# Kernel optimization log

Hardware: AMD Instinct MI355X
Metric: run time of the kernel (lower is better)

Reference implementation:

```python
import jax, jax.numpy as jnp
import numpy as np

NUM_HEADS = 8
DIM_HEAD = 48
SCALE = DIM_HEAD ** -0.5


def setup_inputs() -> dict:
    key = jax.random.key(0)
    k1, k2, k3 = jax.random.split(key, 3)
    B, N, D = 4, 2048, 384
    inner = NUM_HEADS * DIM_HEAD  # 384
    x = jax.random.normal(k1, (B, N, D), dtype=jnp.float32)
    # store weights in [in, out] layout (equivalent to torch Linear W.T)
    Wqkv = jax.random.normal(k2, (D, 3 * inner), dtype=jnp.float32) * (D ** -0.5)
    Wproj = jax.random.normal(k3, (inner, D), dtype=jnp.float32) * (inner ** -0.5)
    bproj = jnp.zeros((D,), dtype=jnp.float32)
    return {"x": x, "Wqkv": Wqkv, "Wproj": Wproj, "bproj": bproj}


def reference(x, Wqkv, Wproj, bproj):
    B, N, D = x.shape
    h, dh = NUM_HEADS, DIM_HEAD
    C = h * dh
    # fused QKV projection (qkv_bias=False)
    qkv = (x @ Wqkv).reshape(B, N, 3, h, dh)
    q = qkv[:, :, 0].transpose(0, 2, 1, 3)  # [B, h, N, dh]
    k = qkv[:, :, 1].transpose(0, 2, 1, 3)
    v = qkv[:, :, 2].transpose(0, 2, 1, 3)
    # naive attention: materialize [B, h, N, N] scores
    sim = jnp.einsum("bhqd,bhkd->bhqk", q, k) * SCALE
    attn = jax.nn.softmax(sim, axis=-1)
    out = jnp.einsum("bhqk,bhkd->bhqd", attn, v)  # [B, h, N, dh]
    out = out.transpose(0, 2, 1, 3).reshape(B, N, C)
    return out @ Wproj + bproj
```

## Files before the change

kernel.cpp:

```cpp
#include <hip/hip_runtime.h>
#include <hip/hip_bf16.h>


typedef _Float16 f16x8 __attribute__((ext_vector_type(8)));
typedef _Float16 f16x4 __attribute__((ext_vector_type(4)));
typedef float    f32x4 __attribute__((ext_vector_type(4)));
typedef float    f32x16 __attribute__((ext_vector_type(16)));

#define QSCL 0.20822035963448658f

__global__ __launch_bounds__(256) void prep(const float* __restrict__ wq,
                                            const float* __restrict__ wp,
                                            _Float16* __restrict__ wqt,
                                            _Float16* __restrict__ wpt)
{
    __shared__ _Float16 t[64][65];
    const int blk = blockIdx.x, tid = threadIdx.x;
    const float* src; _Float16* dst; int Nn, k0, n0;
    if (blk < 108) {
        src = wq; dst = wqt; Nn = 1152;
        k0 = (blk % 6) * 64; n0 = (blk / 6) * 64;
    } else {
        const int b2 = blk - 108;
        src = wp; dst = wpt; Nn = 384;
        k0 = (b2 % 6) * 64; n0 = (b2 / 6) * 64;
    }
    #pragma unroll
    for (int i = 0; i < 16; i++) {
        const int id = tid + i * 256;
        const int k = id >> 6, n = id & 63;
        t[k][n] = (_Float16)src[(size_t)(k0 + k) * Nn + n0 + n];
    }
    __syncthreads();
    #pragma unroll
    for (int i = 0; i < 16; i++) {
        const int id = tid + i * 256;
        const int n = id >> 6, k = id & 63;
        dst[(size_t)(n0 + n) * 384 + k0 + k] = t[k][n];
    }
}

union QkvSmem {
    struct { _Float16 As[128][72]; _Float16 Bs[64][72]; } g;
    _Float16 Ts[64][136];
};

__global__ __launch_bounds__(256) void qkv_f16(const float* __restrict__ X,
                                               const _Float16* __restrict__ Bt,
                                               _Float16* __restrict__ qh,
                                               _Float16* __restrict__ kh,
                                               _Float16* __restrict__ vt)
{
    __shared__ QkvSmem sm;
    const int tid = threadIdx.x;
    const int w = tid >> 6, lane = tid & 63, cl = lane & 15, quad = lane >> 4;
    const int bm = blockIdx.x, bn = blockIdx.y;

    f32x4 acc[2][4];
    const f32x4 z4 = {0.f, 0.f, 0.f, 0.f};
    #pragma unroll
    for (int mi = 0; mi < 2; mi++)
        #pragma unroll
        for (int t = 0; t < 4; t++) acc[mi][t] = z4;

    const int ar = tid >> 3, ac = (tid & 7) * 8;
    const float*    Ag = X  + (size_t)(bm * 128 + ar) * 384 + ac;
    const _Float16* Bg = Bt + (size_t)(bn * 64  + ar) * 384 + ac;

    float4 pa0[4], pa1[4];
    f16x8 pb[2];
    #pragma unroll
    for (int j = 0; j < 4; j++) {
        pa0[j] = *(const float4*)(Ag + (size_t)(32 * j) * 384);
        pa1[j] = *(const float4*)(Ag + (size_t)(32 * j) * 384 + 4);
    }
    #pragma unroll
    for (int j = 0; j < 2; j++) pb[j] = *(const f16x8*)(Bg + (size_t)(32 * j) * 384);

    for (int k0 = 0; k0 < 384; k0 += 64) {
        __syncthreads();
        #pragma unroll
        for (int j = 0; j < 4; j++) {
            f16x8 hh;
            hh[0] = (_Float16)pa0[j].x; hh[1] = (_Float16)pa0[j].y;
            hh[2] = (_Float16)pa0[j].z; hh[3] = (_Float16)pa0[j].w;
            hh[4] = (_Float16)pa1[j].x; hh[5] = (_Float16)pa1[j].y;
            hh[6] = (_Float16)pa1[j].z; hh[7] = (_Float16)pa1[j].w;
            *(f16x8*)&sm.g.As[ar + 32 * j][ac] = hh;
        }
        #pragma unroll
        for (int j = 0; j < 2; j++) *(f16x8*)&sm.g.Bs[ar + 32 * j][ac] = pb[j];
        __syncthreads();
        if (k0 + 64 < 384) {
            #pragma unroll
            for (int j = 0; j < 4; j++) {
                pa0[j] = *(const float4*)(Ag + (size_t)(32 * j) * 384 + k0 + 64);
                pa1[j] = *(const float4*)(Ag + (size_t)(32 * j) * 384 + k0 + 68);
            }
            #pragma unroll
            for (int j = 0; j < 2; j++)
                pb[j] = *(const f16x8*)(Bg + (size_t)(32 * j) * 384 + k0 + 64);
        }
        #pragma unroll
        for (int kh2 = 0; kh2 < 2; kh2++) {
            f16x8 bf[4];
            #pragma unroll
            for (int t = 0; t < 4; t++)
                bf[t] = *(const f16x8*)&sm.g.Bs[t * 16 + cl][kh2 * 32 + quad * 8];
            #pragma unroll
            for (int mi = 0; mi < 2; mi++) {
                const f16x8 af = *(const f16x8*)&sm.g.As[w * 32 + mi * 16 + cl][kh2 * 32 + quad * 8];
                #pragma unroll
                for (int t = 0; t < 4; t++)
                    acc[mi][t] = __builtin_amdgcn_mfma_f32_16x16x32_f16(af, bf[t], acc[mi][t], 0, 0, 0);
            }
        }
    }

    const int s = (bn * 64) / 384;
    if (s == 2) {
        __syncthreads();
        #pragma unroll
        for (int t = 0; t < 4; t++)
            #pragma unroll
            for (int mi = 0; mi < 2; mi++)
                #pragma unroll
                for (int r = 0; r < 4; r++)
                    sm.Ts[t * 16 + cl][w * 32 + mi * 16 + quad * 4 + r] =
                        (_Float16)acc[mi][t][r];
        __syncthreads();
        const int colbase = bn * 64 - 768;
        const int b  = (bm * 128) >> 11;
        const int n0 = (bm * 128) & 2047;
        #pragma unroll
        for (int i = 0; i < 4; i++) {
            const int c = i * 256 + tid;
            const int col = c >> 4, nc = c & 15;
            const int gcol = colbase + col;
            const int head = gcol / 48, d = gcol - head * 48;
            const int bh = b * 8 + head;
            *(f16x8*)&vt[(size_t)(bh * 48 + d) * 2048 + n0 + nc * 8] =
                *(const f16x8*)&sm.Ts[col][nc * 8];
        }
    } else {
        #pragma unroll
        for (int t = 0; t < 4; t++) {
            const int col  = bn * 64 + t * 16 + cl - s * 384;
            const int head = col / 48, d = col - head * 48;
            #pragma unroll
            for (int mi = 0; mi < 2; mi++) {
                #pragma unroll
                for (int r = 0; r < 4; r++) {
                    const int row = bm * 128 + w * 32 + mi * 16 + quad * 4 + r;
                    const int b = row >> 11, n = row & 2047;
                    const int bh = b * 8 + head;
                    const float v = acc[mi][t][r];
                    if (s == 0)
                        qh[(size_t)(bh * 2048 + n) * 48 + d] = (_Float16)(v * QSCL);
                    else
                        kh[(size_t)(bh * 2048 + n) * 48 + d] = (_Float16)v;
                }
            }
        }
    }
}

__global__ __launch_bounds__(256) void attn_f16(const _Float16* __restrict__ qh,
                                                const _Float16* __restrict__ kh,
                                                const _Float16* __restrict__ vt,
                                                _Float16* __restrict__ ab)
{
    __shared__ _Float16 Ks[64][56];
    __shared__ _Float16 Vts[64][72];
    __shared__ _Float16 Ps[128][72];
    const int tid = threadIdx.x;
    const int w = tid >> 6, lane = tid & 63, ln = lane & 31, h = lane >> 5;
    const int bh = blockIdx.x, qt = blockIdx.y;

    for (int i = tid; i < 16 * 72; i += 256) {
        const int r = 48 + i / 72, c = i - (i / 72) * 72;
        Vts[r][c] = (r == 48) ? (_Float16)1.0f : (_Float16)0.0f;
    }

    f16x8 qf[3];
    {
        const _Float16* qp = qh + (size_t)(bh * 2048 + qt * 128 + w * 32 + ln) * 48 + 8 * h;
        qf[0] = *(const f16x8*)qp;
        qf[1] = *(const f16x8*)(qp + 16);
        qf[2] = *(const f16x8*)(qp + 32);
    }

    f32x16 o0, o1;
    #pragma unroll
    for (int r = 0; r < 16; r++) { o0[r] = 0.f; o1[r] = 0.f; }

    const _Float16* kbase = kh + (size_t)bh * 2048 * 48;
    const _Float16* vbase = vt + (size_t)bh * 48 * 2048;

    const int kr0 = tid / 6,         kc0 = (tid % 6) * 8;
    const int kid1 = tid + 256;
    const int kr1 = kid1 / 6,        kc1 = (kid1 % 6) * 8;
    const int vr0 = tid >> 3,        vc0 = (tid & 7) * 8;
    const int vr1 = (tid + 256) >> 3;
    const _Float16* ks0 = kbase + (size_t)kr0 * 48 + kc0;
    const _Float16* ks1 = kbase + (size_t)kr1 * 48 + kc1;
    const _Float16* vs0 = vbase + (size_t)vr0 * 2048 + vc0;
    const _Float16* vs1 = vbase + (size_t)vr1 * 2048 + vc0;

    f16x8 rk0 = *(const f16x8*)ks0;
    f16x8 rv0 = *(const f16x8*)vs0;
    f16x8 rk1, rv1;
    if (tid < 128) { rk1 = *(const f16x8*)ks1; rv1 = *(const f16x8*)vs1; }

    for (int kt = 0; kt < 2048; kt += 64) {
        __syncthreads();
        *(f16x8*)&Ks[kr0][kc0]  = rk0;
        *(f16x8*)&Vts[vr0][vc0] = rv0;
        if (tid < 128) {
            *(f16x8*)&Ks[kr1][kc1]  = rk1;
            *(f16x8*)&Vts[vr1][vc0] = rv1;
        }
        __syncthreads();
        if (kt + 64 < 2048) {
            rk0 = *(const f16x8*)(ks0 + (size_t)(kt + 64) * 48);
            rv0 = *(const f16x8*)(vs0 + kt + 64);
            if (tid < 128) {
                rk1 = *(const f16x8*)(ks1 + (size_t)(kt + 64) * 48);
                rv1 = *(const f16x8*)(vs1 + kt + 64);
            }
        }

        f32x16 s0, s1;
        #pragma unroll
        for (int r = 0; r < 16; r++) { s0[r] = 0.f; s1[r] = 0.f; }
        #pragma unroll
        for (int i = 0; i < 3; i++) {
            const f16x8 ka0 = *(const f16x8*)&Ks[ln][16 * i + 8 * h];
            s0 = __builtin_amdgcn_mfma_f32_32x32x16_f16(ka0, qf[i], s0, 0, 0, 0);
            const f16x8 ka1 = *(const f16x8*)&Ks[32 + ln][16 * i + 8 * h];
            s1 = __builtin_amdgcn_mfma_f32_32x32x16_f16(ka1, qf[i], s1, 0, 0, 0);
        }

        #pragma unroll
        for (int q = 0; q < 4; q++) {
            f16x4 pk;
            pk[0] = (_Float16)exp2f(s0[4 * q + 0]);
            pk[1] = (_Float16)exp2f(s0[4 * q + 1]);
            pk[2] = (_Float16)exp2f(s0[4 * q + 2]);
            pk[3] = (_Float16)exp2f(s0[4 * q + 3]);
            *(f16x4*)&Ps[w * 32 + ln][8 * q + 4 * h] = pk;
            f16x4 pk1;
            pk1[0] = (_Float16)exp2f(s1[4 * q + 0]);
            pk1[1] = (_Float16)exp2f(s1[4 * q + 1]);
            pk1[2] = (_Float16)exp2f(s1[4 * q + 2]);
            pk1[3] = (_Float16)exp2f(s1[4 * q + 3]);
            *(f16x4*)&Ps[w * 32 + ln][32 + 8 * q + 4 * h] = pk1;
        }

        #pragma unroll
        for (int i = 0; i < 4; i++) {
            const f16x8 pa = *(const f16x8*)&Ps[w * 32 + ln][16 * i + 8 * h];
            const f16x8 v0 = *(const f16x8*)&Vts[ln][16 * i + 8 * h];
            o0 = __builtin_amdgcn_mfma_f32_32x32x16_f16(pa, v0, o0, 0, 0, 0);
            const f16x8 v1 = *(const f16x8*)&Vts[32 + ln][16 * i + 8 * h];
            o1 = __builtin_amdgcn_mfma_f32_32x32x16_f16(pa, v1, o1, 0, 0, 0);
        }
    }

    const int b = bh >> 3, hd = bh & 7;
    #pragma unroll
    for (int r = 0; r < 16; r++) {
        const float lr = __shfl(o1[r], (lane & 32) + 16);
        const float inv = 1.f / lr;
        const int q = qt * 128 + w * 32 + (r & 3) + 8 * (r >> 2) + 4 * h;
        _Float16* orow = ab + (size_t)(b * 2048 + q) * 384 + hd * 48;
        orow[ln] = (_Float16)(o0[r] * inv);
        if (ln < 16) orow[32 + ln] = (_Float16)(o1[r] * inv);
    }
}

__global__ __launch_bounds__(256) void proj_f16(const _Float16* __restrict__ A,
                                                const _Float16* __restrict__ Bt,
                                                const float* __restrict__ bias,
                                                float* __restrict__ out)
{
    __shared__ _Float16 As[64][72];
    __shared__ _Float16 Bs[64][72];
    const int tid = threadIdx.x;
    const int w = tid >> 6, lane = tid & 63, cl = lane & 15, quad = lane >> 4;
    const int bm = blockIdx.x, bn = blockIdx.y;

    f32x4 acc[4];
    const f32x4 z4 = {0.f, 0.f, 0.f, 0.f};
    #pragma unroll
    for (int t = 0; t < 4; t++) acc[t] = z4;

    const int ar = tid >> 3, ac = (tid & 7) * 8;
    const _Float16* Ag = A  + (size_t)(bm * 64 + ar) * 384 + ac;
    const _Float16* Bg = Bt + (size_t)(bn * 64 + ar) * 384 + ac;

    f16x8 pa[2], pb[2];
    #pragma unroll
    for (int j = 0; j < 2; j++) {
        pa[j] = *(const f16x8*)(Ag + (size_t)(32 * j) * 384);
        pb[j] = *(const f16x8*)(Bg + (size_t)(32 * j) * 384);
    }

    for (int k0 = 0; k0 < 384; k0 += 64) {
        __syncthreads();
        #pragma unroll
        for (int j = 0; j < 2; j++) {
            *(f16x8*)&As[ar + 32 * j][ac] = pa[j];
            *(f16x8*)&Bs[ar + 32 * j][ac] = pb[j];
        }
        __syncthreads();
        if (k0 + 64 < 384) {
            #pragma unroll
            for (int j = 0; j < 2; j++) {
                pa[j] = *(const f16x8*)(Ag + (size_t)(32 * j) * 384 + k0 + 64);
                pb[j] = *(const f16x8*)(Bg + (size_t)(32 * j) * 384 + k0 + 64);
            }
        }
        #pragma unroll
        for (int kh2 = 0; kh2 < 2; kh2++) {
            const f16x8 af = *(const f16x8*)&As[w * 16 + cl][kh2 * 32 + quad * 8];
            #pragma unroll
            for (int t = 0; t < 4; t++) {
                const f16x8 bf = *(const f16x8*)&Bs[t * 16 + cl][kh2 * 32 + quad * 8];
                acc[t] = __builtin_amdgcn_mfma_f32_16x16x32_f16(af, bf, acc[t], 0, 0, 0);
            }
        }
    }

    #pragma unroll
    for (int t = 0; t < 4; t++) {
        const int col = bn * 64 + t * 16 + cl;
        const float bv = bias[col];
        #pragma unroll
        for (int r = 0; r < 4; r++) {
            const int row = bm * 64 + w * 16 + quad * 4 + r;
            out[(size_t)row * 384 + col] = acc[t][r] + bv;
        }
    }
}

extern "C" void kernel_launch(void* const* d_in, const int* in_sizes, int n_in,
                              void* d_out, int out_size, void* d_ws, size_t ws_size,
                              hipStream_t stream) {
    const float* x     = (const float*)d_in[0];
    const float* Wqkv  = (const float*)d_in[1];
    const float* Wproj = (const float*)d_in[2];
    const float* bproj = (const float*)d_in[3];
    float* out = (float*)d_out;

    char* ws = (char*)d_ws;
    _Float16* wqkvt  = (_Float16*)(ws + 0);
    _Float16* wprojt = (_Float16*)(ws + 884736);
    _Float16* qh     = (_Float16*)(ws + 1179648);
    _Float16* kh     = (_Float16*)(ws + 7471104);
    _Float16* vt     = (_Float16*)(ws + 13762560);
    _Float16* ab     = (_Float16*)(ws + 20054016);

    prep<<<144, 256, 0, stream>>>(Wqkv, Wproj, wqkvt, wprojt);
    qkv_f16<<<dim3(64, 18), 256, 0, stream>>>(x, wqkvt, qh, kh, vt);
    attn_f16<<<dim3(32, 16), 256, 0, stream>>>(qh, kh, vt, ab);
    proj_f16<<<dim3(128, 6), 256, 0, stream>>>(ab, wprojt, bproj, out);
}
```

Baseline: 152.4 us.

## Give each attention wave 64 query rows to reuse K/V fragments

The attention kernel now runs with 128 threads (2 waves) per block instead of 4. Each wave handles 64 query rows as two 32-row groups, so each K fragment and V fragment read from LDS feeds two MFMAs. This cuts LDS read traffic per MFMA and halves the number of waves sharing each block's K/V tile loads. In exchange, register pressure rises (four output accumulators plus two Q sets), per-block parallelism drops, and there are fewer waves per CU to hide latency.

```diff
diff --git a/kernel.cpp b/kernel.cpp
--- a/kernel.cpp
+++ b/kernel.cpp
@@ -165,117 +165,127 @@
     }
 }
 
-__global__ __launch_bounds__(256) void attn_f16(const _Float16* __restrict__ qh,
-                                                const _Float16* __restrict__ kh,
-                                                const _Float16* __restrict__ vt,
-                                                _Float16* __restrict__ ab)
+__global__ __launch_bounds__(128, 1) void attn_f16(const _Float16* __restrict__ qh,
+                                                   const _Float16* __restrict__ kh,
+                                                   const _Float16* __restrict__ vt,
+                                                   _Float16* __restrict__ ab)
 {
     __shared__ _Float16 Ks[64][56];
     __shared__ _Float16 Vts[64][72];
     __shared__ _Float16 Ps[128][72];
     const int tid = threadIdx.x;
-    const int w = tid >> 6, lane = tid & 63, ln = lane & 31, h = lane >> 5;
+    const int wq = tid >> 6, lane = tid & 63, ln = lane & 31, h = lane >> 5;
     const int bh = blockIdx.x, qt = blockIdx.y;
 
-    for (int i = tid; i < 16 * 72; i += 256) {
+    for (int i = tid; i < 16 * 72; i += 128) {
         const int r = 48 + i / 72, c = i - (i / 72) * 72;
         Vts[r][c] = (r == 48) ? (_Float16)1.0f : (_Float16)0.0f;
     }
 
-    f16x8 qf[3];
-    {
-        const _Float16* qp = qh + (size_t)(bh * 2048 + qt * 128 + w * 32 + ln) * 48 + 8 * h;
-        qf[0] = *(const f16x8*)qp;
-        qf[1] = *(const f16x8*)(qp + 16);
-        qf[2] = *(const f16x8*)(qp + 32);
-    }
-
-    f32x16 o0, o1;
-    #pragma unroll
-    for (int r = 0; r < 16; r++) { o0[r] = 0.f; o1[r] = 0.f; }
+    f16x8 qf[2][3];
+    #pragma unroll
+    for (int qg = 0; qg < 2; qg++) {
+        const _Float16* qp = qh + (size_t)(bh * 2048 + qt * 128 + wq * 64 + qg * 32 + ln) * 48 + 8 * h;
+        qf[qg][0] = *(const f16x8*)qp;
+        qf[qg][1] = *(const f16x8*)(qp + 16);
+        qf[qg][2] = *(const f16x8*)(qp + 32);
+    }
+
+    f32x16 o[2][2];
+    #pragma unroll
+    for (int qg = 0; qg < 2; qg++)
+        #pragma unroll
+        for (int cg = 0; cg < 2; cg++)
+            #pragma unroll
+            for (int r = 0; r < 16; r++) o[qg][cg][r] = 0.f;
 
     const _Float16* kbase = kh + (size_t)bh * 2048 * 48;
     const _Float16* vbase = vt + (size_t)bh * 48 * 2048;
 
-    const int kr0 = tid / 6,         kc0 = (tid % 6) * 8;
-    const int kid1 = tid + 256;
-    const int kr1 = kid1 / 6,        kc1 = (kid1 % 6) * 8;
-    const int vr0 = tid >> 3,        vc0 = (tid & 7) * 8;
-    const int vr1 = (tid + 256) >> 3;
-    const _Float16* ks0 = kbase + (size_t)kr0 * 48 + kc0;
-    const _Float16* ks1 = kbase + (size_t)kr1 * 48 + kc1;
-    const _Float16* vs0 = vbase + (size_t)vr0 * 2048 + vc0;
-    const _Float16* vs1 = vbase + (size_t)vr1 * 2048 + vc0;
-
-    f16x8 rk0 = *(const f16x8*)ks0;
-    f16x8 rv0 = *(const f16x8*)vs0;
-    f16x8 rk1, rv1;
-    if (tid < 128) { rk1 = *(const f16x8*)ks1; rv1 = *(const f16x8*)vs1; }
+    int krow[3], kcol[3], vrow[3];
+    const _Float16 *ksp[3], *vsp[3];
+    const int vcol = (tid & 7) * 8;
+    #pragma unroll
+    for (int j = 0; j < 3; j++) {
+        const int c = tid + 128 * j;
+        krow[j] = c / 6;  kcol[j] = (c % 6) * 8;
+        vrow[j] = c >> 3;
+        ksp[j] = kbase + (size_t)krow[j] * 48 + kcol[j];
+        vsp[j] = vbase + (size_t)vrow[j] * 2048 + vcol;
+    }
+    f16x8 rk[3], rv[3];
+    #pragma unroll
+    for (int j = 0; j < 3; j++) { rk[j] = *(const f16x8*)ksp[j]; rv[j] = *(const f16x8*)vsp[j]; }
 
     for (int kt = 0; kt < 2048; kt += 64) {
         __syncthreads();
-        *(f16x8*)&Ks[kr0][kc0]  = rk0;
-        *(f16x8*)&Vts[vr0][vc0] = rv0;
-        if (tid < 128) {
-            *(f16x8*)&Ks[kr1][kc1]  = rk1;
-            *(f16x8*)&Vts[vr1][vc0] = rv1;
+        #pragma unroll
+        for (int j = 0; j < 3; j++) {
+            *(f16x8*)&Ks[krow[j]][kcol[j]] = rk[j];
+            *(f16x8*)&Vts[vrow[j]][vcol]   = rv[j];
         }
         __syncthreads();
         if (kt + 64 < 2048) {
-            rk0 = *(const f16x8*)(ks0 + (size_t)(kt + 64) * 48);
-            rv0 = *(const f16x8*)(vs0 + kt + 64);
-            if (tid < 128) {
-                rk1 = *(const f16x8*)(ks1 + (size_t)(kt + 64) * 48);
-                rv1 = *(const f16x8*)(vs1 + kt + 64);
-            }
-        }
-
-        f32x16 s0, s1;
-        #pragma unroll
-        for (int r = 0; r < 16; r++) { s0[r] = 0.f; s1[r] = 0.f; }
-        #pragma unroll
-        for (int i = 0; i < 3; i++) {
-            const f16x8 ka0 = *(const f16x8*)&Ks[ln][16 * i + 8 * h];
-            s0 = __builtin_amdgcn_mfma_f32_32x32x16_f16(ka0, qf[i], s0, 0, 0, 0);
-            const f16x8 ka1 = *(const f16x8*)&Ks[32 + ln][16 * i + 8 * h];
-            s1 = __builtin_amdgcn_mfma_f32_32x32x16_f16(ka1, qf[i], s1, 0, 0, 0);
-        }
-
-        #pragma unroll
-        for (int q = 0; q < 4; q++) {
-            f16x4 pk;
-            pk[0] = (_Float16)exp2f(s0[4 * q + 0]);
-            pk[1] = (_Float16)exp2f(s0[4 * q + 1]);
-            pk[2] = (_Float16)exp2f(s0[4 * q + 2]);
-            pk[3] = (_Float16)exp2f(s0[4 * q + 3]);
-            *(f16x4*)&Ps[w * 32 + ln][8 * q + 4 * h] = pk;
-            f16x4 pk1;
-            pk1[0] = (_Float16)exp2f(s1[4 * q + 0]);
-            pk1[1] = (_Float16)exp2f(s1[4 * q + 1]);
-            pk1[2] = (_Float16)exp2f(s1[4 * q + 2]);
-            pk1[3] = (_Float16)exp2f(s1[4 * q + 3]);
-            *(f16x4*)&Ps[w * 32 + ln][32 + 8 * q + 4 * h] = pk1;
-        }
-
-        #pragma unroll
-        for (int i = 0; i < 4; i++) {
-            const f16x8 pa = *(const f16x8*)&Ps[w * 32 + ln][16 * i + 8 * h];
-            const f16x8 v0 = *(const f16x8*)&Vts[ln][16 * i + 8 * h];
-            o0 = __builtin_amdgcn_mfma_f32_32x32x16_f16(pa, v0, o0, 0, 0, 0);
-            const f16x8 v1 = *(const f16x8*)&Vts[32 + ln][16 * i + 8 * h];
-            o1 = __builtin_amdgcn_mfma_f32_32x32x16_f16(pa, v1, o1, 0, 0, 0);
+            #pragma unroll
+            for (int j = 0; j < 3; j++) {
+                rk[j] = *(const f16x8*)(ksp[j] + (size_t)(kt + 64) * 48);
+                rv[j] = *(const f16x8*)(vsp[j] + kt + 64);
+            }
+        }
+
+        #pragma unroll
+        for (int kg = 0; kg < 2; kg++) {
+            f32x16 s0, s1;
+            #pragma unroll
+            for (int r = 0; r < 16; r++) { s0[r] = 0.f; s1[r] = 0.f; }
+            #pragma unroll
+            for (int i = 0; i < 3; i++) {
+                const f16x8 ka = *(const f16x8*)&Ks[kg * 32 + ln][16 * i + 8 * h];
+                s0 = __builtin_amdgcn_mfma_f32_32x32x16_f16(ka, qf[0][i], s0, 0, 0, 0);
+                s1 = __builtin_amdgcn_mfma_f32_32x32x16_f16(ka, qf[1][i], s1, 0, 0, 0);
+            }
+            #pragma unroll
+            for (int q = 0; q < 4; q++) {
+                f16x4 pk;
+                pk[0] = (_Float16)exp2f(s0[4 * q + 0]);
+                pk[1] = (_Float16)exp2f(s0[4 * q + 1]);
+                pk[2] = (_Float16)exp2f(s0[4 * q + 2]);
+                pk[3] = (_Float16)exp2f(s0[4 * q + 3]);
+                *(f16x4*)&Ps[wq * 64 + ln][kg * 32 + 8 * q + 4 * h] = pk;
+                f16x4 pk1;
+                pk1[0] = (_Float16)exp2f(s1[4 * q + 0]);
+                pk1[1] = (_Float16)exp2f(s1[4 * q + 1]);
+                pk1[2] = (_Float16)exp2f(s1[4 * q + 2]);
+                pk1[3] = (_Float16)exp2f(s1[4 * q + 3]);
+                *(f16x4*)&Ps[wq * 64 + 32 + ln][kg * 32 + 8 * q + 4 * h] = pk1;
+            }
+        }
+
+        #pragma unroll
+        for (int c = 0; c < 4; c++) {
+            const f16x8 pa0 = *(const f16x8*)&Ps[wq * 64 + ln][16 * c + 8 * h];
+            const f16x8 pa1 = *(const f16x8*)&Ps[wq * 64 + 32 + ln][16 * c + 8 * h];
+            const f16x8 bv0 = *(const f16x8*)&Vts[ln][16 * c + 8 * h];
+            const f16x8 bv1 = *(const f16x8*)&Vts[32 + ln][16 * c + 8 * h];
+            o[0][0] = __builtin_amdgcn_mfma_f32_32x32x16_f16(pa0, bv0, o[0][0], 0, 0, 0);
+            o[0][1] = __builtin_amdgcn_mfma_f32_32x32x16_f16(pa0, bv1, o[0][1], 0, 0, 0);
+            o[1][0] = __builtin_amdgcn_mfma_f32_32x32x16_f16(pa1, bv0, o[1][0], 0, 0, 0);
+            o[1][1] = __builtin_amdgcn_mfma_f32_32x32x16_f16(pa1, bv1, o[1][1], 0, 0, 0);
         }
     }
 
     const int b = bh >> 3, hd = bh & 7;
     #pragma unroll
-    for (int r = 0; r < 16; r++) {
-        const float lr = __shfl(o1[r], (lane & 32) + 16);
-        const float inv = 1.f / lr;
-        const int q = qt * 128 + w * 32 + (r & 3) + 8 * (r >> 2) + 4 * h;
-        _Float16* orow = ab + (size_t)(b * 2048 + q) * 384 + hd * 48;
-        orow[ln] = (_Float16)(o0[r] * inv);
-        if (ln < 16) orow[32 + ln] = (_Float16)(o1[r] * inv);
+    for (int qg = 0; qg < 2; qg++) {
+        #pragma unroll
+        for (int r = 0; r < 16; r++) {
+            const float lr = __shfl(o[qg][1][r], (lane & 32) + 16);
+            const float inv = 1.f / lr;
+            const int q = qt * 128 + wq * 64 + qg * 32 + (r & 3) + 8 * (r >> 2) + 4 * h;
+            _Float16* orow = ab + (size_t)(b * 2048 + q) * 384 + hd * 48;
+            orow[ln] = (_Float16)(o[qg][0][r] * inv);
+            if (ln < 16) orow[32 + ln] = (_Float16)(o[qg][1][r] * inv);
+        }
     }
 }
 
@@ -363,6 +373,6 @@
 
     prep<<<144, 256, 0, stream>>>(Wqkv, Wproj, wqkvt, wprojt);
     qkv_f16<<<dim3(64, 18), 256, 0, stream>>>(x, wqkvt, qh, kh, vt);
-    attn_f16<<<dim3(32, 16), 256, 0, stream>>>(qh, kh, vt, ab);
+    attn_f16<<<dim3(32, 16), 128, 0, stream>>>(qh, kh, vt, ab);
     proj_f16<<<dim3(128, 6), 256, 0, stream>>>(ab, wprojt, bproj, out);
 }
```

Result: slower. 192.1 us (+26.1%).
